# Performance work log

Measured on AMD Instinct MI355X. Metric: run time of the kernel, lower is better.

Reference implementation:

```python
import jax, jax.numpy as jnp
import numpy as np

B, T, C, H = 4, 2048, 1024, 16
D = C // H  # head_dim = 64


def setup_inputs() -> dict:
    key = jax.random.key(0)
    ks = jax.random.split(key, 10)
    s = 1.0 / np.sqrt(C)
    inp = {
        "x": jax.random.normal(ks[0], (B, T, C), dtype=jnp.float32),
        "attention_mask": jnp.ones((B, T), dtype=jnp.int32),
        "Wq": jax.random.normal(ks[1], (C, C), dtype=jnp.float32) * s,
        "bq": jnp.zeros((C,), dtype=jnp.float32),
        "Wk": jax.random.normal(ks[2], (C, C), dtype=jnp.float32) * s,
        "bk": jnp.zeros((C,), dtype=jnp.float32),
        "Wv": jax.random.normal(ks[3], (C, C), dtype=jnp.float32) * s,
        "bv": jnp.zeros((C,), dtype=jnp.float32),
        "Wp": jax.random.normal(ks[4], (C, C), dtype=jnp.float32) * s,
        "bp": jnp.zeros((C,), dtype=jnp.float32),
    }
    return inp


def reference(x, attention_mask, Wq, bq, Wk, bk, Wv, bv, Wp, bp):
    # x: [B,T,C] -> q,k,v: [B,H,T,D]
    def heads(y):
        return y.reshape(B, T, H, D).transpose(0, 2, 1, 3)

    q = heads(x @ Wq + bq)
    k = heads(x @ Wk + bk)
    v = heads(x @ Wv + bv)

    scale = 1.0 / np.sqrt(D)
    att = jnp.einsum("bhqd,bhkd->bhqk", q, k) * scale  # [B,H,T,T]

    causal = jnp.tril(jnp.ones((T, T), dtype=bool))  # [T,T]
    mask = causal[None, None, :, :] & (attention_mask[:, None, None, :] != 0)
    att = jnp.where(mask, att, -jnp.inf)
    att = jax.nn.softmax(att, axis=-1)
    # dropout is identity in eval mode

    y = jnp.einsum("bhqk,bhkd->bhqd", att, v)  # [B,H,T,D]
    y = y.transpose(0, 2, 1, 3).reshape(B, T, C)
    return y @ Wp + bp
```

## Files before the change

kernel.cpp:

```cpp
#include <hip/hip_runtime.h>

#define BB 4
#define TT 2048
#define CC 1024
#define HH 16
#define DD 64

typedef unsigned short u16;
typedef unsigned int u32;
typedef __bf16 bf16;
typedef __attribute__((ext_vector_type(8))) bf16 bf16x8;
typedef __attribute__((ext_vector_type(8))) u16 u16x8;
typedef __attribute__((ext_vector_type(4))) u16 u16x4;
typedef __attribute__((ext_vector_type(4))) float f32x4;

static __device__ __forceinline__ u16 f2b(float f) {
  unsigned u = __builtin_bit_cast(unsigned, f);
  u += 0x7fffu + ((u >> 16) & 1u);
  return (u16)(u >> 16);
}
static __device__ __forceinline__ u16 bfc(float f) {
  return __builtin_bit_cast(u16, (__bf16)f);
}

__global__ void cvt_bf16_kernel(const float* __restrict__ src, u16* __restrict__ dst, int n8) {
  int i = blockIdx.x * blockDim.x + threadIdx.x;
  if (i >= n8) return;
  const float4* p4 = reinterpret_cast<const float4*>(src) + (size_t)i * 2;
  float4 a = p4[0], b = p4[1];
  u16x8 o;
  o[0] = f2b(a.x); o[1] = f2b(a.y); o[2] = f2b(a.z); o[3] = f2b(a.w);
  o[4] = f2b(b.x); o[5] = f2b(b.y); o[6] = f2b(b.z); o[7] = f2b(b.w);
  *reinterpret_cast<u16x8*>(dst + (size_t)i * 8) = o;
}

__global__ void transp_w_kernel(const float* __restrict__ w0, const float* __restrict__ w1,
                                const float* __restrict__ w2, const float* __restrict__ w3,
                                u16* __restrict__ wqkvT, u16* __restrict__ wpT) {
  __shared__ float t[32][33];
  int z = blockIdx.z;
  const float* src = z == 0 ? w0 : z == 1 ? w1 : z == 2 ? w2 : w3;
  u16* dst = z < 3 ? wqkvT + (size_t)z * CC * CC : wpT;
  int k0 = blockIdx.x * 32, n0 = blockIdx.y * 32;
  int tx = threadIdx.x & 31, ty = threadIdx.x >> 5;
#pragma unroll
  for (int i = 0; i < 4; ++i)
    t[ty + i * 8][tx] = src[(size_t)(k0 + ty + i * 8) * CC + n0 + tx];
  __syncthreads();
#pragma unroll
  for (int i = 0; i < 4; ++i)
    dst[(size_t)(n0 + ty + i * 8) * CC + k0 + tx] = f2b(t[tx][ty + i * 8]);
}

__global__ void mask_prep_kernel(const int* __restrict__ am, float* __restrict__ gm,
                                 u32* __restrict__ fwords) {
  __shared__ u32 sf[32];
  int b = blockIdx.x;
  int lane = threadIdx.x & 63, w = threadIdx.x >> 6;
#pragma unroll
  for (int j = 0; j < 8; ++j) {
    int c = w * 8 + j;
    int i = c * 64 + lane;
    int v = am[b * TT + i];
    gm[b * TT + i] = v ? 0.f : -1e30f;
    unsigned long long bal = __ballot(v != 0);
    if (lane == 0) sf[c] = (bal == ~0ull) ? 1u : 0u;
  }
  __syncthreads();
  if (threadIdx.x == 0) {
    u32 fw = 0;
    for (int c = 0; c < 32; ++c) fw |= sf[c] << c;
    fwords[b] = fw;
  }
}

template <int MODE>
__global__ __launch_bounds__(256) void gemm_bt_kernel(
    const u16* __restrict__ A, const u16* __restrict__ Bt, int K, int N,
    const float* __restrict__ b0, const float* __restrict__ b1, const float* __restrict__ b2,
    u16* __restrict__ q_out, u16* __restrict__ k_out, u16* __restrict__ v_out,
    float* __restrict__ f_out) {
  __shared__ u16 As[128 * 32];
  __shared__ u16 Bs[128 * 32];
  const int tid = threadIdx.x, lane = tid & 63, w = tid >> 6;
  const int wm = w >> 1, wn = w & 1;
  const int m0 = blockIdx.x * 128, n0 = blockIdx.y * 128;
  const int lrow = lane >> 2, lcol = (lane & 3) * 8;
  f32x4 acc[4][4] = {};

  for (int k0 = 0; k0 < K; k0 += 32) {
    if (k0) __syncthreads();
#pragma unroll
    for (int r = 0; r < 2; ++r) {
      int row = r * 64 + w * 16 + lrow;
      __builtin_amdgcn_global_load_lds(
          (const __attribute__((address_space(1))) void*)(A + (size_t)(m0 + row) * K + k0 + lcol),
          (__attribute__((address_space(3))) void*)(As + (r * 64 + w * 16) * 32),
          16, 0, 0);
      __builtin_amdgcn_global_load_lds(
          (const __attribute__((address_space(1))) void*)(Bt + (size_t)(n0 + row) * K + k0 + lcol),
          (__attribute__((address_space(3))) void*)(Bs + (r * 64 + w * 16) * 32),
          16, 0, 0);
    }
    __syncthreads();
    bf16x8 af[4], bfr[4];
#pragma unroll
    for (int i = 0; i < 4; ++i) {
      af[i] = *reinterpret_cast<const bf16x8*>(&As[(wm * 64 + i * 16 + (lane & 15)) * 32 + (lane >> 4) * 8]);
      bfr[i] = *reinterpret_cast<const bf16x8*>(&Bs[(wn * 64 + i * 16 + (lane & 15)) * 32 + (lane >> 4) * 8]);
    }
#pragma unroll
    for (int i = 0; i < 4; ++i)
#pragma unroll
      for (int j = 0; j < 4; ++j)
        acc[i][j] = __builtin_amdgcn_mfma_f32_16x16x32_bf16(af[i], bfr[j], acc[i][j], 0, 0, 0);
  }

  const int mrow = m0 + wm * 64;
  const int ncol = n0 + wn * 64;
  if (MODE == 0) {
    const int g = n0 >> 10;
    const float* bias = g == 0 ? b0 : g == 1 ? b1 : b2;
    if (g < 2) {
      u16* dst = g == 0 ? q_out : k_out;
      const float scl = (g == 0) ? 0.18033688f : 1.0f;
#pragma unroll
      for (int i = 0; i < 4; ++i)
#pragma unroll
        for (int j = 0; j < 4; ++j)
#pragma unroll
          for (int r = 0; r < 4; ++r) {
            int m = mrow + i * 16 + (lane >> 4) * 4 + r;
            int n = ncol + j * 16 + (lane & 15);
            float v = (acc[i][j][r] + bias[n & 1023]) * scl;
            int b = m >> 11, t = m & 2047;
            int h = (n >> 6) & 15, d = n & 63;
            dst[(((size_t)(b * HH + h)) * TT + t) * DD + d] = f2b(v);
          }
    } else {
#pragma unroll
      for (int i = 0; i < 4; ++i)
#pragma unroll
        for (int j = 0; j < 4; ++j) {
          int n = ncol + j * 16 + (lane & 15);
          int h = (n >> 6) & 15, d = n & 63;
          float bias_v = bias[n & 1023];
          int mb = mrow + i * 16 + (lane >> 4) * 4;
          int b = mb >> 11, t = mb & 2047;
          u16x4 vv;
#pragma unroll
          for (int r = 0; r < 4; ++r) vv[r] = f2b(acc[i][j][r] + bias_v);
          *reinterpret_cast<u16x4*>(v_out + (((size_t)(b * HH + h)) * DD + d) * TT + t) = vv;
        }
    }
  } else {
#pragma unroll
    for (int i = 0; i < 4; ++i)
#pragma unroll
      for (int j = 0; j < 4; ++j)
#pragma unroll
        for (int r = 0; r < 4; ++r) {
          int m = mrow + i * 16 + (lane >> 4) * 4 + r;
          int n = ncol + j * 16 + (lane & 15);
          f_out[(size_t)m * N + n] = acc[i][j][r] + b0[n];
        }
  }
}

__global__ __launch_bounds__(256, 2) void attn_kernel(
    const u16* __restrict__ Q, const u16* __restrict__ K, const u16* __restrict__ Vt,
    const float* __restrict__ gm, const u32* __restrict__ fwords, u16* __restrict__ Y) {
  __shared__ __align__(16) char LDS[51200];
  const int flat = blockIdx.x;
  const int xcd = flat & 7, idx = flat >> 3;
  const int bh = xcd * 8 + (idx & 7);
  const int jb = 15 - (idx >> 3);
  const int b = bh >> 4, h = bh & 15;
  const int tid = threadIdx.x, lane = tid & 63, w = tid >> 6;
  const int lq = lane & 15, g = lane >> 4;
  const int qt = 4 * jb + w;
  const int q0 = qt * 32;
  const int nkt = (qt >> 1) + 1;
  const int nktm = 2 * jb + 2;
  const u32 fw = fwords[b];

  const u16* Qb = Q + (size_t)bh * TT * DD;
  const char* Kb = (const char*)(K + (size_t)bh * TT * DD);
  const char* Vb = (const char*)(Vt + (size_t)bh * DD * TT);

  const int l3 = lane >> 3, l7 = lane & 7;
  const int swb = (l7 * 16) ^ (l3 << 4);
  const char* kp0 = Kb + (2 * w + 0) * 1024 + l3 * 128 + swb;
  const char* kp1 = Kb + (2 * w + 1) * 1024 + l3 * 128 + swb;
  const char* vp0 = Vb + (size_t)((2 * w + 0) * 8 + l3) * 4096 + swb;
  const char* vp1 = Vb + (size_t)((2 * w + 1) * 8 + l3) * 4096 + swb;

  const int sw2 = (lq & 7) << 4;
  const int fb0 = lq * 128 + ((g * 16) ^ sw2);
  const int fb1 = lq * 128 + (((64) + g * 16) ^ sw2);
  const int pwb = 32768 + w * 4608 + lq * 144 + g * 8;
  const int prb = 32768 + w * 4608 + lq * 144 + g * 16;

  auto STAGE = [&](int buf, int kt2) {
    const int ko = kt2 * 8192, vo = kt2 * 128, lb = buf * 8192;
    __builtin_amdgcn_global_load_lds(
        (const __attribute__((address_space(1))) void*)(kp0 + ko),
        (__attribute__((address_space(3))) void*)(LDS + lb + (2 * w + 0) * 1024), 16, 0, 0);
    __builtin_amdgcn_global_load_lds(
        (const __attribute__((address_space(1))) void*)(kp1 + ko),
        (__attribute__((address_space(3))) void*)(LDS + lb + (2 * w + 1) * 1024), 16, 0, 0);
    __builtin_amdgcn_global_load_lds(
        (const __attribute__((address_space(1))) void*)(vp0 + vo),
        (__attribute__((address_space(3))) void*)(LDS + 16384 + lb + (2 * w + 0) * 1024), 16, 0, 0);
    __builtin_amdgcn_global_load_lds(
        (const __attribute__((address_space(1))) void*)(vp1 + vo),
        (__attribute__((address_space(3))) void*)(LDS + 16384 + lb + (2 * w + 1) * 1024), 16, 0, 0);
  };

  bf16x8 qf[2][2];
#pragma unroll
  for (int n = 0; n < 2; ++n)
#pragma unroll
    for (int ks = 0; ks < 2; ++ks)
      qf[n][ks] = *reinterpret_cast<const bf16x8*>(
          Qb + (size_t)(q0 + n * 16 + lq) * DD + ks * 32 + g * 8);

  f32x4 o[4][2] = {};
  float mrun[2] = {-1e30f, -1e30f};
  float lrun[2] = {0.f, 0.f};
  const f32x4 z4 = {0.f, 0.f, 0.f, 0.f};

  STAGE(0, 0);
  STAGE(1, 1);

  auto TILE = [&](int BUF, int kt) {
    if (kt < nktm - 1)
      asm volatile("s_waitcnt vmcnt(4)" ::: "memory");
    else
      asm volatile("s_waitcnt vmcnt(0)" ::: "memory");
    asm volatile("s_barrier" ::: "memory");

    if (kt < nkt) {
      const int kv0 = kt * 64;
      bf16x8 kf0[4], kf1[4];
#pragma unroll
      for (int m = 0; m < 4; ++m) {
        kf0[m] = *reinterpret_cast<const bf16x8*>(LDS + BUF * 8192 + m * 2048 + fb0);
        kf1[m] = *reinterpret_cast<const bf16x8*>(LDS + BUF * 8192 + m * 2048 + fb1);
      }
      f32x4 s[4][2];
      __builtin_amdgcn_s_setprio(1);
#pragma unroll
      for (int m = 0; m < 4; ++m)
#pragma unroll
        for (int n = 0; n < 2; ++n) {
          s[m][n] = __builtin_amdgcn_mfma_f32_16x16x32_bf16(kf0[m], qf[n][0], z4, 0, 0, 0);
          s[m][n] = __builtin_amdgcn_mfma_f32_16x16x32_bf16(kf1[m], qf[n][1], s[m][n], 0, 0, 0);
        }
      __builtin_amdgcn_s_setprio(0);

      if (!((fw >> kt) & 1u)) {
#pragma unroll
        for (int m = 0; m < 4; ++m) {
          float4 mv = *reinterpret_cast<const float4*>(gm + b * TT + kv0 + m * 16 + g * 4);
#pragma unroll
          for (int n = 0; n < 2; ++n) {
            s[m][n][0] += mv.x; s[m][n][1] += mv.y;
            s[m][n][2] += mv.z; s[m][n][3] += mv.w;
          }
        }
      }
      if (kt == nkt - 1) {
#pragma unroll
        for (int n = 0; n < 2; ++n) {
          const int q = q0 + n * 16 + lq;
#pragma unroll
          for (int m = 0; m < 4; ++m)
#pragma unroll
            for (int r = 0; r < 4; ++r) {
              int kv = kv0 + m * 16 + g * 4 + r;
              s[m][n][r] = (kv <= q) ? s[m][n][r] : -1e30f;
            }
        }
      }

#pragma unroll
      for (int n = 0; n < 2; ++n) {
        float rm = fmaxf(fmaxf(fmaxf(s[0][n][0], s[0][n][1]), fmaxf(s[0][n][2], s[0][n][3])),
                         fmaxf(fmaxf(s[1][n][0], s[1][n][1]), fmaxf(s[1][n][2], s[1][n][3])));
        float rm2 = fmaxf(fmaxf(fmaxf(s[2][n][0], s[2][n][1]), fmaxf(s[2][n][2], s[2][n][3])),
                          fmaxf(fmaxf(s[3][n][0], s[3][n][1]), fmaxf(s[3][n][2], s[3][n][3])));
        rm = fmaxf(rm, rm2);
        if (!__all(rm <= mrun[n] + 8.f)) {
          float rg = fmaxf(rm, __shfl_xor(rm, 16));
          rg = fmaxf(rg, __shfl_xor(rg, 32));
          float mnew = fmaxf(mrun[n], rg);
          float corr = __builtin_exp2f(mrun[n] - mnew);
          mrun[n] = mnew;
          lrun[n] *= corr;
#pragma unroll
          for (int nd = 0; nd < 4; ++nd)
#pragma unroll
            for (int r = 0; r < 4; ++r) o[nd][n][r] *= corr;
        }
        const float mn = mrun[n];
        float rs = 0.f;
#pragma unroll
        for (int m = 0; m < 4; ++m) {
          float p0 = __builtin_exp2f(s[m][n][0] - mn);
          float p1 = __builtin_exp2f(s[m][n][1] - mn);
          float p2 = __builtin_exp2f(s[m][n][2] - mn);
          float p3 = __builtin_exp2f(s[m][n][3] - mn);
          rs += (p0 + p1) + (p2 + p3);
          u32 wa, wb;
          asm("v_cvt_pk_bf16_f32 %0, %1, %2" : "=v"(wa) : "v"(p0), "v"(p1));
          asm("v_cvt_pk_bf16_f32 %0, %1, %2" : "=v"(wb) : "v"(p2), "v"(p3));
          uint2 pw; pw.x = wa; pw.y = wb;
          *reinterpret_cast<uint2*>(LDS + pwb + n * 2304 + m * 32) = pw;
        }
        lrun[n] += rs;
      }

      asm volatile("s_waitcnt lgkmcnt(0)" ::: "memory");
      __builtin_amdgcn_sched_barrier(0);

      __builtin_amdgcn_s_setprio(1);
#pragma unroll
      for (int ks = 0; ks < 2; ++ks) {
        const int fb = ks ? fb1 : fb0;
        bf16x8 pf0 = *reinterpret_cast<const bf16x8*>(LDS + prb + 0 * 2304 + ks * 64);
        bf16x8 pf1 = *reinterpret_cast<const bf16x8*>(LDS + prb + 1 * 2304 + ks * 64);
#pragma unroll
        for (int nd = 0; nd < 4; ++nd) {
          bf16x8 vf = *reinterpret_cast<const bf16x8*>(LDS + 16384 + BUF * 8192 + nd * 2048 + fb);
          o[nd][0] = __builtin_amdgcn_mfma_f32_16x16x32_bf16(vf, pf0, o[nd][0], 0, 0, 0);
          o[nd][1] = __builtin_amdgcn_mfma_f32_16x16x32_bf16(vf, pf1, o[nd][1], 0, 0, 0);
        }
      }
      __builtin_amdgcn_s_setprio(0);
    }

    asm volatile("s_barrier" ::: "memory");
    if (kt + 2 < nktm) STAGE(BUF, kt + 2);
  };

  for (int kt = 0; kt < nktm; kt += 2) {
    TILE(0, kt);
    TILE(1, kt + 1);
  }

#pragma unroll
  for (int n = 0; n < 2; ++n) {
    float l = lrun[n];
    l += __shfl_xor(l, 16);
    l += __shfl_xor(l, 32);
    float inv = 1.0f / l;
    const int q = q0 + n * 16 + lq;
#pragma unroll
    for (int nd = 0; nd < 4; ++nd) {
      u16x4 yv;
#pragma unroll
      for (int r = 0; r < 4; ++r) yv[r] = bfc(o[nd][n][r] * inv);
      *reinterpret_cast<u16x4*>(
          Y + ((size_t)(b * TT + q)) * CC + h * DD + nd * 16 + g * 4) = yv;
    }
  }
}

extern "C" void kernel_launch(void* const* d_in, const int* in_sizes, int n_in,
                              void* d_out, int out_size, void* d_ws, size_t ws_size,
                              hipStream_t stream) {
  const float* x  = (const float*)d_in[0];
  const int*   am = (const int*)d_in[1];
  const float* Wq = (const float*)d_in[2];
  const float* bq = (const float*)d_in[3];
  const float* Wk = (const float*)d_in[4];
  const float* bk = (const float*)d_in[5];
  const float* Wv = (const float*)d_in[6];
  const float* bv = (const float*)d_in[7];
  const float* Wp = (const float*)d_in[8];
  const float* bp = (const float*)d_in[9];
  float* out = (float*)d_out;

  char* ws = (char*)d_ws;
  u16* xb    = (u16*)(ws);
  u16* wqkvT = (u16*)(ws + (16ull << 20));
  u16* wpT   = (u16*)(ws + (22ull << 20));
  u16* qw    = (u16*)(ws + (24ull << 20));
  u16* kw    = (u16*)(ws + (40ull << 20));
  u16* vw    = (u16*)(ws + (56ull << 20));
  u16* yb    = (u16*)(ws + (72ull << 20));
  float* gm  = (float*)d_out;
  u32* fwords = (u32*)((char*)d_out + (64ull << 10));

  mask_prep_kernel<<<dim3(BB), 256, 0, stream>>>(am, gm, fwords);
  {
    int n8 = BB * TT * CC / 8;
    cvt_bf16_kernel<<<n8 / 256, 256, 0, stream>>>(x, xb, n8);
  }
  transp_w_kernel<<<dim3(32, 32, 4), 256, 0, stream>>>(Wq, Wk, Wv, Wp, wqkvT, wpT);
  gemm_bt_kernel<0><<<dim3(64, 24), 256, 0, stream>>>(
      xb, wqkvT, CC, 3 * CC, bq, bk, bv, qw, kw, vw, nullptr);
  attn_kernel<<<dim3(1024), 256, 0, stream>>>(qw, kw, vw, gm, fwords, yb);
  gemm_bt_kernel<1><<<dim3(64, 8), 256, 0, stream>>>(
      yb, wpT, CC, CC, bp, nullptr, nullptr, nullptr, nullptr, nullptr, out);
}
```

Before: 193.2 us.

## Double-buffer GEMMs with 256x256 swizzled-LDS tile for QKV projection

Replaces the single generic GEMM with two specialized kernels. The QKV GEMM now uses 512-thread blocks computing 256x256 tiles with 64-wide K steps, XOR-swizzled LDS to avoid bank conflicts, and a two-stage global_load_lds pipeline with explicit vmcnt waits. The output projection GEMM keeps 128x128 tiles but gains double buffering and s_setprio around the MFMA blocks. The aim is to hide load latency and raise data reuse per LDS byte. In exchange it uses 128KB of LDS per block, which limits occupancy, and the QKV grid shrinks to 384 blocks.

Result: faster. 186.2 us (-3.6%).

```diff
diff --git a/kernel.cpp b/kernel.cpp
--- a/kernel.cpp
+++ b/kernel.cpp
@@ -74,97 +74,199 @@
   }
 }
 
-template <int MODE>
-__global__ __launch_bounds__(256) void gemm_bt_kernel(
-    const u16* __restrict__ A, const u16* __restrict__ Bt, int K, int N,
-    const float* __restrict__ b0, const float* __restrict__ b1, const float* __restrict__ b2,
-    u16* __restrict__ q_out, u16* __restrict__ k_out, u16* __restrict__ v_out,
-    float* __restrict__ f_out) {
-  __shared__ u16 As[128 * 32];
-  __shared__ u16 Bs[128 * 32];
+__global__ __launch_bounds__(512, 2) void qkv_gemm_kernel(
+    const u16* __restrict__ A, const u16* __restrict__ Bt,
+    const float* __restrict__ bq, const float* __restrict__ bk, const float* __restrict__ bv,
+    u16* __restrict__ q_out, u16* __restrict__ k_out, u16* __restrict__ v_out) {
+  __shared__ __align__(16) char LDS[131072];
+  const int tid = threadIdx.x, lane = tid & 63, w = tid >> 6;
+  const int wm = w >> 2, wn = w & 3;
+  const int lq = lane & 15, g = lane >> 4;
+  const int m0 = blockIdx.x * 256, n0 = blockIdx.y * 256;
+
+  const int l3 = lane >> 3;
+  const int swb = ((lane & 7) ^ (l3 & 7)) * 16;
+  const char* pS[8];
+#pragma unroll
+  for (int h = 0; h < 2; ++h)
+#pragma unroll
+    for (int r = 0; r < 2; ++r) {
+      int row = h * 128 + r * 64 + w * 8 + l3;
+      pS[h * 2 + r]     = (const char*)A  + (size_t)(m0 + row) * 2048 + swb;
+      pS[4 + h * 2 + r] = (const char*)Bt + (size_t)(n0 + row) * 2048 + swb;
+    }
+
+  auto STAGE = [&](int db, int t) {
+    const int off = t * 128;
+#pragma unroll
+    for (int m = 0; m < 2; ++m)
+#pragma unroll
+      for (int h = 0; h < 2; ++h)
+#pragma unroll
+        for (int r = 0; r < 2; ++r)
+          __builtin_amdgcn_global_load_lds(
+              (const __attribute__((address_space(1))) void*)(pS[m * 4 + h * 2 + r] + off),
+              (__attribute__((address_space(3))) void*)(
+                  LDS + m * 65536 + db * 32768 + h * 16384 + r * 8192 + w * 1024),
+              16, 0, 0);
+  };
+
+  const int acol0 = (g * 16) ^ ((lq & 7) << 4);
+  const int acol1 = (64 + g * 16) ^ ((lq & 7) << 4);
+  const int aBase = wm * 16384 + lq * 128;
+  const int bBase = 65536 + (wn >> 1) * 16384 + ((wn & 1) * 64 + lq) * 128;
+
+  f32x4 acc[8][4] = {};
+
+  auto TILE = [&](int db, int t) {
+    if (t == 15)
+      asm volatile("s_waitcnt vmcnt(0)" ::: "memory");
+    else
+      asm volatile("s_waitcnt vmcnt(8)" ::: "memory");
+    asm volatile("s_barrier" ::: "memory");
+    const char* la = LDS + db * 32768 + aBase;
+    const char* lb = LDS + db * 32768 + bBase;
+#pragma unroll
+    for (int i4 = 0; i4 < 2; ++i4) {
+      bf16x8 af[4][2];
+#pragma unroll
+      for (int i = 0; i < 4; ++i) {
+        af[i][0] = *reinterpret_cast<const bf16x8*>(la + (i4 * 4 + i) * 2048 + acol0);
+        af[i][1] = *reinterpret_cast<const bf16x8*>(la + (i4 * 4 + i) * 2048 + acol1);
+      }
+#pragma unroll
+      for (int j2 = 0; j2 < 2; ++j2) {
+        bf16x8 bfr[2][2];
+#pragma unroll
+        for (int j = 0; j < 2; ++j) {
+          bfr[j][0] = *reinterpret_cast<const bf16x8*>(lb + (j2 * 2 + j) * 2048 + acol0);
+          bfr[j][1] = *reinterpret_cast<const bf16x8*>(lb + (j2 * 2 + j) * 2048 + acol1);
+        }
+        __builtin_amdgcn_s_setprio(1);
+#pragma unroll
+        for (int i = 0; i < 4; ++i)
+#pragma unroll
+          for (int j = 0; j < 2; ++j) {
+            f32x4& a = acc[i4 * 4 + i][j2 * 2 + j];
+            a = __builtin_amdgcn_mfma_f32_16x16x32_bf16(af[i][0], bfr[j][0], a, 0, 0, 0);
+            a = __builtin_amdgcn_mfma_f32_16x16x32_bf16(af[i][1], bfr[j][1], a, 0, 0, 0);
+          }
+        __builtin_amdgcn_s_setprio(0);
+      }
+    }
+    asm volatile("s_barrier" ::: "memory");
+    if (t + 2 < 16) STAGE(db, t + 2);
+  };
+
+  STAGE(0, 0);
+  STAGE(1, 1);
+  for (int t = 0; t < 16; t += 2) {
+    TILE(0, t);
+    TILE(1, t + 1);
+  }
+
+  const int g3 = n0 >> 10;
+  const int mrow = m0 + wm * 128;
+  const int ncol = n0 + wn * 64;
+  if (g3 < 2) {
+    u16* dst = g3 == 0 ? q_out : k_out;
+    const float* bias = g3 == 0 ? bq : bk;
+    const float scl = g3 == 0 ? 0.18033688f : 1.0f;
+#pragma unroll
+    for (int i = 0; i < 8; ++i)
+#pragma unroll
+      for (int j = 0; j < 4; ++j) {
+        int n = ncol + j * 16 + lq;
+        int h = (n >> 6) & 15, d = n & 63;
+        float bb = bias[n & 1023];
+#pragma unroll
+        for (int r = 0; r < 4; ++r) {
+          int m = mrow + i * 16 + g * 4 + r;
+          int b = m >> 11, t = m & 2047;
+          dst[(((size_t)(b * HH + h)) * TT + t) * DD + d] = f2b((acc[i][j][r] + bb) * scl);
+        }
+      }
+  } else {
+#pragma unroll
+    for (int i = 0; i < 8; ++i)
+#pragma unroll
+      for (int j = 0; j < 4; ++j) {
+        int n = ncol + j * 16 + lq;
+        int h = (n >> 6) & 15, d = n & 63;
+        float bb = bv[n & 1023];
+        int mb = mrow + i * 16 + g * 4;
+        int b = mb >> 11, t = mb & 2047;
+        u16x4 vv;
+#pragma unroll
+        for (int r = 0; r < 4; ++r) vv[r] = f2b(acc[i][j][r] + bb);
+        *reinterpret_cast<u16x4*>(v_out + (((size_t)(b * HH + h)) * DD + d) * TT + t) = vv;
+      }
+  }
+}
+
+__global__ __launch_bounds__(256) void proj_gemm_kernel(
+    const u16* __restrict__ A, const u16* __restrict__ Bt,
+    const float* __restrict__ bias, float* __restrict__ f_out) {
+  __shared__ u16 As[2][128 * 32];
+  __shared__ u16 Bs[2][128 * 32];
   const int tid = threadIdx.x, lane = tid & 63, w = tid >> 6;
   const int wm = w >> 1, wn = w & 1;
   const int m0 = blockIdx.x * 128, n0 = blockIdx.y * 128;
   const int lrow = lane >> 2, lcol = (lane & 3) * 8;
   f32x4 acc[4][4] = {};
 
-  for (int k0 = 0; k0 < K; k0 += 32) {
-    if (k0) __syncthreads();
+  auto STAGE = [&](int db, int kt) {
+    const int k0 = kt * 32;
 #pragma unroll
     for (int r = 0; r < 2; ++r) {
       int row = r * 64 + w * 16 + lrow;
       __builtin_amdgcn_global_load_lds(
-          (const __attribute__((address_space(1))) void*)(A + (size_t)(m0 + row) * K + k0 + lcol),
-          (__attribute__((address_space(3))) void*)(As + (r * 64 + w * 16) * 32),
-          16, 0, 0);
+          (const __attribute__((address_space(1))) void*)(A + (size_t)(m0 + row) * CC + k0 + lcol),
+          (__attribute__((address_space(3))) void*)(&As[db][(r * 64 + w * 16) * 32]), 16, 0, 0);
       __builtin_amdgcn_global_load_lds(
-          (const __attribute__((address_space(1))) void*)(Bt + (size_t)(n0 + row) * K + k0 + lcol),
-          (__attribute__((address_space(3))) void*)(Bs + (r * 64 + w * 16) * 32),
-          16, 0, 0);
+          (const __attribute__((address_space(1))) void*)(Bt + (size_t)(n0 + row) * CC + k0 + lcol),
+          (__attribute__((address_space(3))) void*)(&Bs[db][(r * 64 + w * 16) * 32]), 16, 0, 0);
     }
-    __syncthreads();
+  };
+
+  STAGE(0, 0);
+  STAGE(1, 1);
+  for (int kt = 0; kt < 32; ++kt) {
+    if (kt == 31)
+      asm volatile("s_waitcnt vmcnt(0)" ::: "memory");
+    else
+      asm volatile("s_waitcnt vmcnt(4)" ::: "memory");
+    asm volatile("s_barrier" ::: "memory");
+    const int db = kt & 1;
     bf16x8 af[4], bfr[4];
 #pragma unroll
     for (int i = 0; i < 4; ++i) {
-      af[i] = *reinterpret_cast<const bf16x8*>(&As[(wm * 64 + i * 16 + (lane & 15)) * 32 + (lane >> 4) * 8]);
-      bfr[i] = *reinterpret_cast<const bf16x8*>(&Bs[(wn * 64 + i * 16 + (lane & 15)) * 32 + (lane >> 4) * 8]);
+      af[i] = *reinterpret_cast<const bf16x8*>(&As[db][(wm * 64 + i * 16 + (lane & 15)) * 32 + (lane >> 4) * 8]);
+      bfr[i] = *reinterpret_cast<const bf16x8*>(&Bs[db][(wn * 64 + i * 16 + (lane & 15)) * 32 + (lane >> 4) * 8]);
     }
+    __builtin_amdgcn_s_setprio(1);
 #pragma unroll
     for (int i = 0; i < 4; ++i)
 #pragma unroll
       for (int j = 0; j < 4; ++j)
         acc[i][j] = __builtin_amdgcn_mfma_f32_16x16x32_bf16(af[i], bfr[j], acc[i][j], 0, 0, 0);
+    __builtin_amdgcn_s_setprio(0);
+    asm volatile("s_barrier" ::: "memory");
+    if (kt + 2 < 32) STAGE(db, kt + 2);
   }
 
   const int mrow = m0 + wm * 64;
   const int ncol = n0 + wn * 64;
-  if (MODE == 0) {
-    const int g = n0 >> 10;
-    const float* bias = g == 0 ? b0 : g == 1 ? b1 : b2;
-    if (g < 2) {
-      u16* dst = g == 0 ? q_out : k_out;
-      const float scl = (g == 0) ? 0.18033688f : 1.0f;
-#pragma unroll
-      for (int i = 0; i < 4; ++i)
-#pragma unroll
-        for (int j = 0; j < 4; ++j)
-#pragma unroll
-          for (int r = 0; r < 4; ++r) {
-            int m = mrow + i * 16 + (lane >> 4) * 4 + r;
-            int n = ncol + j * 16 + (lane & 15);
-            float v = (acc[i][j][r] + bias[n & 1023]) * scl;
-            int b = m >> 11, t = m & 2047;
-            int h = (n >> 6) & 15, d = n & 63;
-            dst[(((size_t)(b * HH + h)) * TT + t) * DD + d] = f2b(v);
-          }
-    } else {
-#pragma unroll
-      for (int i = 0; i < 4; ++i)
-#pragma unroll
-        for (int j = 0; j < 4; ++j) {
-          int n = ncol + j * 16 + (lane & 15);
-          int h = (n >> 6) & 15, d = n & 63;
-          float bias_v = bias[n & 1023];
-          int mb = mrow + i * 16 + (lane >> 4) * 4;
-          int b = mb >> 11, t = mb & 2047;
-          u16x4 vv;
-#pragma unroll
-          for (int r = 0; r < 4; ++r) vv[r] = f2b(acc[i][j][r] + bias_v);
-          *reinterpret_cast<u16x4*>(v_out + (((size_t)(b * HH + h)) * DD + d) * TT + t) = vv;
-        }
-    }
-  } else {
-#pragma unroll
-    for (int i = 0; i < 4; ++i)
-#pragma unroll
-      for (int j = 0; j < 4; ++j)
-#pragma unroll
-        for (int r = 0; r < 4; ++r) {
-          int m = mrow + i * 16 + (lane >> 4) * 4 + r;
-          int n = ncol + j * 16 + (lane & 15);
-          f_out[(size_t)m * N + n] = acc[i][j][r] + b0[n];
-        }
-  }
+#pragma unroll
+  for (int i = 0; i < 4; ++i)
+#pragma unroll
+    for (int j = 0; j < 4; ++j)
+#pragma unroll
+      for (int r = 0; r < 4; ++r) {
+        int m = mrow + i * 16 + (lane >> 4) * 4 + r;
+        int n = ncol + j * 16 + (lane & 15);
+        f_out[(size_t)m * CC + n] = acc[i][j][r] + bias[n];
+      }
 }
 
 __global__ __launch_bounds__(256, 2) void attn_kernel(
@@ -399,9 +501,8 @@
     cvt_bf16_kernel<<<n8 / 256, 256, 0, stream>>>(x, xb, n8);
   }
   transp_w_kernel<<<dim3(32, 32, 4), 256, 0, stream>>>(Wq, Wk, Wv, Wp, wqkvT, wpT);
-  gemm_bt_kernel<0><<<dim3(64, 24), 256, 0, stream>>>(
-      xb, wqkvT, CC, 3 * CC, bq, bk, bv, qw, kw, vw, nullptr);
+  qkv_gemm_kernel<<<dim3(32, 12), 512, 0, stream>>>(
+      xb, wqkvT, bq, bk, bv, qw, kw, vw);
   attn_kernel<<<dim3(1024), 256, 0, stream>>>(qw, kw, vw, gm, fwords, yb);
-  gemm_bt_kernel<1><<<dim3(64, 8), 256, 0, stream>>>(
-      yb, wpT, CC, CC, bp, nullptr, nullptr, nullptr, nullptr, nullptr, out);
-}
+  proj_gemm_kernel<<<dim3(64, 8), 256, 0, stream>>>(yb, wpT, bp, out);
+}
```
